# Performance work log

Measured on AMD Instinct MI355X. Metric: run time of the kernel, lower is better.

The kernel has to match this reference:

```python
import jax, jax.numpy as jnp
import numpy as np

N, HID, L, NC = 2048, 256, 4, 10
D0, D1, D2 = HID, HID // 2, HID // 8   # dims for degrees l=0,1,2
H, DH = 4, HID // 4                    # heads for degree-0 attention
F = D0 + D1 + D2                       # invariant feature width
C2 = float(np.sqrt(3.0))


def setup_inputs() -> dict:
    key = jax.random.key(0)
    ks = jax.random.split(key, 16)

    def w(k, shape, fan):
        return jax.random.normal(k, shape, jnp.float32) / np.float32(np.sqrt(fan))

    return {
        "x": jax.random.uniform(ks[0], (N, 118), jnp.float32),
        "pos": jax.random.normal(ks[1], (N, 3), jnp.float32) * 3.0,
        "emb_W": w(ks[2], (118, D0), 118),
        "emb_b": jnp.zeros((D0,), jnp.float32),
        "Wq": w(ks[3], (L, F, H * DH), F),
        "Wk": w(ks[4], (L, F, H * DH), F),
        "Wv0": w(ks[5], (L, D0, D0), D0),
        "Wv1": w(ks[6], (L, D1, D1), D1),
        "Wv2": w(ks[7], (L, D2, D2), D2),
        "Ws1": w(ks[8], (L, D0, D1), D0),
        "Ws2": w(ks[9], (L, D0, D2), D0),
        "Wffa": w(ks[10], (L, D0, 2 * D0), D0),
        "Wffb": w(ks[11], (L, 2 * D0, D0), 2 * D0),
        "Wg": w(ks[12], (L, F, D1 + D2), F),
        "out_W": w(ks[13], (D0, NC), D0),
        "out_b": jnp.zeros((NC,), jnp.float32),
    }


def _sph_harmonics(pos):
    """Real spherical harmonics Y1 [N,N,3], Y2 [N,N,5] of pairwise unit vectors."""
    rel = pos[None, :, :] - pos[:, None, :]                  # [N,N,3]
    dist = jnp.linalg.norm(rel, axis=-1, keepdims=True)
    valid = (dist > 1e-6).astype(pos.dtype)                  # zero out self-pairs
    u = rel / jnp.maximum(dist, 1e-6) * valid
    ux, uy, uz = u[..., 0], u[..., 1], u[..., 2]
    Y1 = u
    Y2 = jnp.stack([
        C2 * ux * uy,
        C2 * uy * uz,
        0.5 * (3.0 * uz * uz - 1.0),
        C2 * ux * uz,
        0.5 * C2 * (ux * ux - uy * uy),
    ], axis=-1) * valid                                      # [N,N,5]
    return Y1, Y2


def _invariants(x0, x1, x2):
    return jnp.concatenate([
        x0,
        jnp.linalg.norm(x1, axis=-1),
        jnp.linalg.norm(x2, axis=-1),
    ], axis=-1)                                              # [N,F]


def _layer(x0, x1, x2, Y1, Y2, Wq, Wk, Wv0, Wv1, Wv2, Ws1, Ws2, Wffa, Wffb, Wg):
    inv = _invariants(x0, x1, x2)
    q = (inv @ Wq).reshape(N, H, DH)
    k = (inv @ Wk).reshape(N, H, DH)
    attn = jax.nn.softmax(jnp.einsum('nhd,mhd->hnm', q, k) / np.float32(np.sqrt(DH)), axis=-1)

    # degree-0 aggregation (4 heads)
    v0 = (x0 @ Wv0).reshape(N, H, D0 // H)
    agg0 = jnp.einsum('hnm,mhc->nhc', attn, v0).reshape(N, D0)

    a = attn.mean(0)                                         # [N,N] single head for l>0
    # degree-1: channel-mixed values + degree-0 -> degree-1 via Y1
    v1 = jnp.einsum('mdc,de->mec', x1, Wv1)                  # [N,D1,3]
    agg1 = jnp.einsum('nm,mdc->ndc', a, v1)
    mix1 = jnp.einsum('nmc,md->ndc', a[:, :, None] * Y1, x0 @ Ws1)
    # degree-2: channel-mixed values + degree-0 -> degree-2 via Y2
    v2 = jnp.einsum('mdc,de->mec', x2, Wv2)                  # [N,D2,5]
    agg2 = jnp.einsum('nm,mdc->ndc', a, v2)
    mix2 = jnp.einsum('nmc,md->ndc', a[:, :, None] * Y2, x0 @ Ws2)

    x0 = x0 + agg0
    x1 = x1 + agg1 + mix1
    x2 = x2 + agg2 + mix2

    # gated equivariant feedforward
    x0 = x0 + jax.nn.silu(x0 @ Wffa) @ Wffb
    g = jax.nn.sigmoid(_invariants(x0, x1, x2) @ Wg)         # [N,D1+D2]
    x1 = x1 * g[:, :D1, None]
    x2 = x2 * g[:, D1:, None]
    return x0, x1, x2


def reference(x, pos, emb_W, emb_b, Wq, Wk, Wv0, Wv1, Wv2, Ws1, Ws2, Wffa, Wffb, Wg, out_W, out_b):
    Y1, Y2 = _sph_harmonics(pos)
    x0 = x @ emb_W + emb_b                                   # input embedding
    x1 = jnp.zeros((N, D1, 3), x0.dtype)
    x2 = jnp.zeros((N, D2, 5), x0.dtype)
    for l in range(L):
        x0, x1, x2 = _layer(x0, x1, x2, Y1, Y2,
                            Wq[l], Wk[l], Wv0[l], Wv1[l], Wv2[l],
                            Ws1[l], Ws2[l], Wffa[l], Wffb[l], Wg[l])
    return x0 @ out_W + out_b                                # [N, num_classes]
```

## Files before the change

### kernel.cpp

```cpp
#include <hip/hip_runtime.h>
#include <math.h>

#define N_    2048
#define D0_   256
#define D1_   128
#define D2_   32
#define F_    416
#define H_    4
#define DH_   64
#define L_    4
#define NC_   10
#define C2_   1.7320508075688772f
#define X12W  544

typedef unsigned short u16;
typedef __attribute__((ext_vector_type(8))) short short8v;
typedef __attribute__((ext_vector_type(4))) float f32x4;

union U8 { u16 u[8]; short8v v; };

__device__ __forceinline__ u16 f2bf(float f) {
    union { float f; unsigned int u; } x; x.f = f;
    unsigned int r = x.u + 0x7FFFu + ((x.u >> 16) & 1u);
    return (u16)(r >> 16);
}
__device__ __forceinline__ float bf2f(u16 u) {
    union { float f; unsigned int u; } x; x.u = ((unsigned int)u) << 16;
    return x.f;
}

__device__ __forceinline__ f32x4 mfma16(short8v a, short8v b, f32x4 c) {
    return __builtin_amdgcn_mfma_f32_16x16x32_bf16(a, b, c, 0, 0, 0);
}

enum { B_NN = 0, B_NT = 1 };
enum { EPI_STORE = 0, EPI_SILU = 1, EPI_SIGMOID = 2, EPI_ACCUM = 3, EPI_ATOMIC = 4,
       EPI_STOREB = 5 };

template<int BLAY, int EPI>
__global__ __launch_bounds__(256) void mfma_gemm(
    const float* __restrict__ A, int lda,
    const float* __restrict__ B, int ldb,
    const float* __restrict__ bias,
    float* __restrict__ C, int ldc,
    int M, int K, int Nn, float scale, int kchunk,
    int zk, long long Ah, long long Bh, long long Ch)
{
    __shared__ __align__(16) u16 As[64][40];
    __shared__ __align__(16) u16 Bs[64][40];
    const int t = threadIdx.x;
    const int bm = blockIdx.y * 64, bn = blockIdx.x * 64;
    const int hz = blockIdx.z / zk, kz = blockIdx.z % zk;
    A += (size_t)hz * Ah; B += (size_t)hz * Bh;
    const int lane = t & 63, w = t >> 6;
    const int r0 = (w >> 1) * 32, c0 = (w & 1) * 32;
    const int fr = lane & 15, fk = (lane >> 4) * 8;
    const int ml = t >> 2, k8 = (t & 3) * 8;
    const int kbeg = kz * kchunk;
    const int kend = (kbeg + kchunk < K) ? kbeg + kchunk : K;
    f32x4 acc[2][2] = {};

    for (int k0 = kbeg; k0 < kend; k0 += 32) {
        {
            U8 u;
            if (((lda & 3) == 0) && (k0 + 32 <= kend)) {
                const float* ap = A + (size_t)(bm + ml) * lda + k0 + k8;
                float4 a0 = *(const float4*)ap;
                float4 a1 = *(const float4*)(ap + 4);
                u.u[0]=f2bf(a0.x); u.u[1]=f2bf(a0.y); u.u[2]=f2bf(a0.z); u.u[3]=f2bf(a0.w);
                u.u[4]=f2bf(a1.x); u.u[5]=f2bf(a1.y); u.u[6]=f2bf(a1.z); u.u[7]=f2bf(a1.w);
            } else {
#pragma unroll
                for (int j = 0; j < 8; ++j) {
                    int kk = k0 + k8 + j;
                    u.u[j] = f2bf(kk < kend ? A[(size_t)(bm + ml) * lda + kk] : 0.f);
                }
            }
            *(short8v*)&As[ml][k8] = u.v;
        }
        {
            U8 u;
            if (BLAY == B_NT) {
                if (((ldb & 3) == 0) && (k0 + 32 <= kend) && (bn + ml < Nn)) {
                    const float* bp = B + (size_t)(bn + ml) * ldb + k0 + k8;
                    float4 b0 = *(const float4*)bp;
                    float4 b1 = *(const float4*)(bp + 4);
                    u.u[0]=f2bf(b0.x); u.u[1]=f2bf(b0.y); u.u[2]=f2bf(b0.z); u.u[3]=f2bf(b0.w);
                    u.u[4]=f2bf(b1.x); u.u[5]=f2bf(b1.y); u.u[6]=f2bf(b1.z); u.u[7]=f2bf(b1.w);
                } else {
#pragma unroll
                    for (int j = 0; j < 8; ++j) {
                        int kk = k0 + k8 + j;
                        u.u[j] = f2bf((kk < kend && bn + ml < Nn)
                                      ? B[(size_t)(bn + ml) * ldb + kk] : 0.f);
                    }
                }
            } else {
                int nc = bn + ml;
#pragma unroll
                for (int j = 0; j < 8; ++j) {
                    int kk = k0 + k8 + j;
                    u.u[j] = f2bf((kk < kend && nc < Nn) ? B[(size_t)kk * ldb + nc] : 0.f);
                }
            }
            *(short8v*)&Bs[ml][k8] = u.v;
        }
        __syncthreads();
        short8v a0 = *(const short8v*)&As[r0 + fr][fk];
        short8v a1 = *(const short8v*)&As[r0 + 16 + fr][fk];
        short8v b0 = *(const short8v*)&Bs[c0 + fr][fk];
        short8v b1 = *(const short8v*)&Bs[c0 + 16 + fr][fk];
        acc[0][0] = mfma16(a0, b0, acc[0][0]);
        acc[0][1] = mfma16(a0, b1, acc[0][1]);
        acc[1][0] = mfma16(a1, b0, acc[1][0]);
        acc[1][1] = mfma16(a1, b1, acc[1][1]);
        __syncthreads();
    }
#pragma unroll
    for (int mi = 0; mi < 2; ++mi)
#pragma unroll
    for (int ni = 0; ni < 2; ++ni)
#pragma unroll
    for (int r = 0; r < 4; ++r) {
        int row = bm + r0 + mi * 16 + ((lane >> 4) << 2) + r;
        int col = bn + c0 + ni * 16 + fr;
        if (col >= Nn) continue;
        float v = acc[mi][ni][r];
        if (EPI == EPI_STOREB) {
            ((u16*)C + (size_t)hz * Ch)[(size_t)row * ldc + col] = f2bf(v * scale);
        } else {
            float* cp = C + (size_t)hz * Ch + (size_t)row * ldc + col;
            if (EPI == EPI_STORE)   *cp = v * scale + (bias ? bias[col] : 0.f);
            if (EPI == EPI_SILU)    *cp = v / (1.f + expf(-v));
            if (EPI == EPI_SIGMOID) *cp = 1.f / (1.f + expf(-v));
            if (EPI == EPI_ACCUM)   *cp += v;
            if (EPI == EPI_ATOMIC)  atomicAdd(cp, v);
        }
    }
}

__global__ __launch_bounds__(256) void transpose_bf16(
    const float* __restrict__ in, u16* __restrict__ outT, int R, int C)
{
    __shared__ float tile[64][65];
    const int br = blockIdx.y * 64, bc = blockIdx.x * 64;
    const int t = threadIdx.x, lc = t & 63, q = t >> 6;
#pragma unroll 4
    for (int r = 0; r < 16; ++r) {
        int row = br + q * 16 + r, col = bc + lc;
        tile[q * 16 + r][lc] = (col < C) ? in[(size_t)row * C + col] : 0.f;
    }
    __syncthreads();
#pragma unroll 4
    for (int r = 0; r < 16; ++r) {
        int orow = bc + q * 16 + r;
        int ocol = br + lc;
        if (orow < C) outT[(size_t)orow * R + ocol] = f2bf(tile[lc][q * 16 + r]);
    }
}

template<int NB>
__global__ __launch_bounds__(256) void aggP(
    const u16* __restrict__ A, int lda,
    const u16* __restrict__ BT, int ldk,
    float* __restrict__ C, int ldc,
    int K, int Nn, int kchunk,
    int zk, long long Ah, long long Bh, long long Ch)
{
    __shared__ __align__(16) u16 As[64][40];
    __shared__ __align__(16) u16 Bs[NB][64][40];
    const int t = threadIdx.x;
    const int bm = blockIdx.y * 64, bn0 = blockIdx.x * 64 * NB;
    const int hz = blockIdx.z / zk, kz = blockIdx.z % zk;
    A += (size_t)hz * Ah; BT += (size_t)hz * Bh; C += (size_t)hz * Ch;
    const int lane = t & 63, w = t >> 6;
    const int r0 = (w >> 1) * 32, c0 = (w & 1) * 32;
    const int fr = lane & 15, fk = (lane >> 4) * 8;
    const int ml = t >> 2, k8 = (t & 3) * 8;
    const int kbeg = kz * kchunk;
    const int kend = (kbeg + kchunk < K) ? kbeg + kchunk : K;
    f32x4 acc[NB][2][2] = {};

    for (int k0 = kbeg; k0 < kend; k0 += 32) {
        *(short8v*)&As[ml][k8] = *(const short8v*)(A + (size_t)(bm + ml) * lda + k0 + k8);
#pragma unroll
        for (int nb = 0; nb < NB; ++nb) {
            int nc = bn0 + nb * 64 + ml;
            short8v z = {};
            *(short8v*)&Bs[nb][ml][k8] = (nc < Nn)
                ? *(const short8v*)(BT + (size_t)nc * ldk + k0 + k8) : z;
        }
        __syncthreads();
        short8v a0 = *(const short8v*)&As[r0 + fr][fk];
        short8v a1 = *(const short8v*)&As[r0 + 16 + fr][fk];
#pragma unroll
        for (int nb = 0; nb < NB; ++nb) {
            short8v b0 = *(const short8v*)&Bs[nb][c0 + fr][fk];
            short8v b1 = *(const short8v*)&Bs[nb][c0 + 16 + fr][fk];
            acc[nb][0][0] = mfma16(a0, b0, acc[nb][0][0]);
            acc[nb][0][1] = mfma16(a0, b1, acc[nb][0][1]);
            acc[nb][1][0] = mfma16(a1, b0, acc[nb][1][0]);
            acc[nb][1][1] = mfma16(a1, b1, acc[nb][1][1]);
        }
        __syncthreads();
    }
#pragma unroll
    for (int nb = 0; nb < NB; ++nb)
#pragma unroll
    for (int mi = 0; mi < 2; ++mi)
#pragma unroll
    for (int ni = 0; ni < 2; ++ni)
#pragma unroll
    for (int r = 0; r < 4; ++r) {
        int row = bm + r0 + mi * 16 + ((lane >> 4) << 2) + r;
        int col = bn0 + nb * 64 + c0 + ni * 16 + fr;
        if (col >= Nn) continue;
        atomicAdd(C + (size_t)row * ldc + col, acc[nb][mi][ni][r]);
    }
}

__global__ void ucompute_kernel(const float* __restrict__ pos, u16* __restrict__ U) {
    int idx = blockIdx.x * 256 + threadIdx.x;
    int n = idx >> 11, m = idx & (N_ - 1);
    float rx = pos[m * 3 + 0] - pos[n * 3 + 0];
    float ry = pos[m * 3 + 1] - pos[n * 3 + 1];
    float rz = pos[m * 3 + 2] - pos[n * 3 + 2];
    float d2 = rx * rx + ry * ry + rz * rz;
    bool valid = d2 > 1e-12f;
    float rinv = valid ? rsqrtf(d2) : 0.f;
    size_t base = (size_t)n * N_ + m;
    const size_t CS = (size_t)N_ * N_;
    U[base]          = f2bf(rx * rinv);
    U[base + CS]     = f2bf(ry * rinv);
    U[base + 2 * CS] = f2bf(rz * rinv);
}

__global__ __launch_bounds__(256) void mixc_kernel(
    const u16* __restrict__ amb, const u16* __restrict__ U,
    const u16* __restrict__ s1T, const u16* __restrict__ s2T,
    float* __restrict__ Macc)
{
    const int ch = blockIdx.z;
    const int gx = blockIdx.x;
    const bool deg1 = ch < 3;
    if (!deg1 && gx >= 8) return;
    const int bm = blockIdx.y * 64;
    const size_t CS = (size_t)N_ * N_;
    const int colbase = deg1 ? (gx & 1) * 64 : 0;
    const int ks      = deg1 ? (gx >> 1) : gx;
    const u16* BT     = deg1 ? s1T : s2T;
    __shared__ __align__(16) u16 As[64][40];
    __shared__ __align__(16) u16 Bs[64][40];
    const int t = threadIdx.x, lane = t & 63, w = t >> 6;
    const int r0 = (w >> 1) * 32, c0 = (w & 1) * 32;
    const int fr = lane & 15, fk = (lane >> 4) * 8;
    const int ml = t >> 2, k8 = (t & 3) * 8;
    const int kbeg = ks * 256, kend = kbeg + 256;
    f32x4 acc[2][2] = {};

    for (int m0 = kbeg; m0 < kend; m0 += 32) {
        const size_t off = (size_t)(bm + ml) * N_ + m0 + k8;
        U8 am8; am8.v = *(const short8v*)(amb + off);
        U8 o;
        if (deg1) {
            U8 uv; uv.v = *(const short8v*)(U + (size_t)ch * CS + off);
#pragma unroll
            for (int j = 0; j < 8; ++j)
                o.u[j] = f2bf(bf2f(am8.u[j]) * bf2f(uv.u[j]));
        } else {
            U8 xv, yv, zv;
            xv.v = *(const short8v*)(U + off);
            yv.v = *(const short8v*)(U + CS + off);
            zv.v = *(const short8v*)(U + 2 * CS + off);
#pragma unroll
            for (int j = 0; j < 8; ++j) {
                float a = bf2f(am8.u[j]);
                float ux = bf2f(xv.u[j]), uy = bf2f(yv.u[j]), uz = bf2f(zv.u[j]);
                float y;
                if      (ch == 3) y = C2_ * ux * uy;
                else if (ch == 4) y = C2_ * uy * uz;
                else if (ch == 5) y = (ux*ux + uy*uy + uz*uz > 0.5f)
                                      ? 0.5f * (3.f * uz * uz - 1.f) : 0.f;
                else if (ch == 6) y = C2_ * ux * uz;
                else              y = 0.5f * C2_ * (ux * ux - uy * uy);
                o.u[j] = f2bf(a * y);
            }
        }
        *(short8v*)&As[ml][k8] = o.v;
        {
            int nc = colbase + ml;
            short8v z = {};
            *(short8v*)&Bs[ml][k8] = (deg1 || nc < 32)
                ? *(const short8v*)(BT + (size_t)nc * N_ + m0 + k8) : z;
        }
        __syncthreads();
        short8v a0 = *(const short8v*)&As[r0 + fr][fk];
        short8v a1 = *(const short8v*)&As[r0 + 16 + fr][fk];
        short8v b0 = *(const short8v*)&Bs[c0 + fr][fk];
        short8v b1 = *(const short8v*)&Bs[c0 + 16 + fr][fk];
        acc[0][0] = mfma16(a0, b0, acc[0][0]);
        acc[0][1] = mfma16(a0, b1, acc[0][1]);
        acc[1][0] = mfma16(a1, b0, acc[1][0]);
        acc[1][1] = mfma16(a1, b1, acc[1][1]);
        __syncthreads();
    }
#pragma unroll
    for (int mi = 0; mi < 2; ++mi)
#pragma unroll
    for (int ni = 0; ni < 2; ++ni)
#pragma unroll
    for (int r = 0; r < 4; ++r) {
        int row = bm + r0 + mi * 16 + ((lane >> 4) << 2) + r;
        int col = colbase + c0 + ni * 16 + fr;
        float v = acc[mi][ni][r];
        if (deg1)
            atomicAdd(&Macc[(size_t)ch * N_ * 128 + (size_t)row * 128 + col], v);
        else if (col < 32)
            atomicAdd(&Macc[(size_t)3 * N_ * 128 + (size_t)(ch - 3) * N_ * 32
                            + (size_t)row * 32 + col], v);
    }
}

__global__ void mix_combine(const float* __restrict__ Macc, float* __restrict__ x12) {
    int idx = blockIdx.x * 256 + threadIdx.x;
    if (idx >= N_ * X12W) return;
    int n = idx / X12W, j = idx % X12W;
    float v;
    if (j < 384) {
        int e = j / 3, c = j - 3 * e;
        v = Macc[(size_t)c * N_ * 128 + (size_t)n * 128 + e];
    } else {
        int jj = j - 384;
        int e = jj / 5, c = jj - 5 * e;
        v = Macc[(size_t)3 * N_ * 128 + (size_t)c * N_ * 32 + (size_t)n * 32 + e];
    }
    x12[idx] += v;
}

__global__ void invar_kernel(const float* __restrict__ x0, const float* __restrict__ x12,
                             float* __restrict__ inv) {
    int n = blockIdx.x, t = threadIdx.x;
    inv[(size_t)n * F_ + t] = x0[(size_t)n * D0_ + t];
    if (t < 128) {
        const float* p = x12 + (size_t)n * X12W + t * 3;
        inv[(size_t)n * F_ + 256 + t] = sqrtf(p[0]*p[0] + p[1]*p[1] + p[2]*p[2]);
    }
    if (t < 32) {
        const float* p = x12 + (size_t)n * X12W + 384 + t * 5;
        inv[(size_t)n * F_ + 384 + t] =
            sqrtf(p[0]*p[0] + p[1]*p[1] + p[2]*p[2] + p[3]*p[3] + p[4]*p[4]);
    }
}

__global__ void v1_kernel(const float* __restrict__ x12, const float* __restrict__ W,
                          float* __restrict__ Vflat) {
    int m = blockIdx.x, t = threadIdx.x;
    __shared__ float sh[384];
    sh[t] = x12[(size_t)m * X12W + t];
    __syncthreads();
    int e = t / 3, c = t % 3;
    float acc = 0.f;
#pragma unroll 4
    for (int d = 0; d < 128; ++d)
        acc = fmaf(sh[d * 3 + c], W[d * 128 + e], acc);
    Vflat[(size_t)m * X12W + t] = acc;
}

__global__ void v2_kernel(const float* __restrict__ x12, const float* __restrict__ W,
                          float* __restrict__ Vflat) {
    int m = blockIdx.x, t = threadIdx.x;
    __shared__ float sh[160];
    if (t < 160) sh[t] = x12[(size_t)m * X12W + 384 + t];
    __syncthreads();
    if (t < 160) {
        int e = t / 5, c = t % 5;
        float acc = 0.f;
#pragma unroll 4
        for (int d = 0; d < 32; ++d)
            acc = fmaf(sh[d * 5 + c], W[d * 32 + e], acc);
        Vflat[(size_t)m * X12W + 384 + t] = acc;
    }
}

__global__ void softmax4(u16* __restrict__ Sb, u16* __restrict__ amb) {
    int n = blockIdx.x, t = threadIdx.x;
    __shared__ float red[256];
    const size_t NN = (size_t)N_ * N_;
    float amv[8] = {};
    for (int h = 0; h < H_; ++h) {
        u16* Sp = Sb + (size_t)h * NN + (size_t)n * N_ + t * 8;
        U8 sv; sv.v = *(const short8v*)Sp;
        float s[8];
#pragma unroll
        for (int j = 0; j < 8; ++j) s[j] = bf2f(sv.u[j]);
        float mx = s[0];
#pragma unroll
        for (int j = 1; j < 8; ++j) mx = fmaxf(mx, s[j]);
        red[t] = mx; __syncthreads();
        for (int st = 128; st > 0; st >>= 1) { if (t < st) red[t] = fmaxf(red[t], red[t + st]); __syncthreads(); }
        mx = red[0]; __syncthreads();
        float sum = 0.f;
#pragma unroll
        for (int j = 0; j < 8; ++j) { s[j] = expf(s[j] - mx); sum += s[j]; }
        red[t] = sum; __syncthreads();
        for (int st = 128; st > 0; st >>= 1) { if (t < st) red[t] += red[t + st]; __syncthreads(); }
        float rinv = 1.f / red[0]; __syncthreads();
        U8 pv;
#pragma unroll
        for (int j = 0; j < 8; ++j) {
            float p = s[j] * rinv;
            pv.u[j] = f2bf(p);
            amv[j] += 0.25f * p;
        }
        *(short8v*)Sp = pv.v;
    }
    U8 av;
#pragma unroll
    for (int j = 0; j < 8; ++j) av.u[j] = f2bf(amv[j]);
    *(short8v*)(amb + (size_t)n * N_ + t * 8) = av.v;
}

__global__ void gate_kernel(const float* __restrict__ g, float* __restrict__ x12) {
    int idx = blockIdx.x * 256 + threadIdx.x;
    if (idx >= N_ * X12W) return;
    int n = idx / X12W, j = idx % X12W;
    float gv = (j < 384) ? g[n * 160 + j / 3] : g[n * 160 + 128 + (j - 384) / 5];
    x12[idx] *= gv;
}

extern "C" void kernel_launch(void* const* d_in, const int* in_sizes, int n_in,
                              void* d_out, int out_size, void* d_ws, size_t ws_size,
                              hipStream_t stream) {
    const float* x    = (const float*)d_in[0];
    const float* pos  = (const float*)d_in[1];
    const float* embW = (const float*)d_in[2];
    const float* embB = (const float*)d_in[3];
    const float* Wq   = (const float*)d_in[4];
    const float* Wk   = (const float*)d_in[5];
    const float* Wv0  = (const float*)d_in[6];
    const float* Wv1  = (const float*)d_in[7];
    const float* Wv2  = (const float*)d_in[8];
    const float* Ws1  = (const float*)d_in[9];
    const float* Ws2  = (const float*)d_in[10];
    const float* Wffa = (const float*)d_in[11];
    const float* Wffb = (const float*)d_in[12];
    const float* Wg   = (const float*)d_in[13];
    const float* outW = (const float*)d_in[14];
    const float* outB = (const float*)d_in[15];
    float* out = (float*)d_out;

    const size_t NN = (size_t)N_ * N_;
    float* p = (float*)d_ws;
    float* x0    = p; p += N_ * D0_;
    float* x12   = p; p += N_ * X12W;
    float* inv   = p; p += N_ * F_;
    float* q     = p; p += N_ * D0_;
    float* k     = p; p += N_ * D0_;
    float* v0    = p; p += N_ * D0_;
    float* Vflat = p; p += N_ * X12W;
    float* s1    = p; p += N_ * D1_;
    float* s2    = p; p += N_ * D2_;
    float* fft   = p; p += N_ * 512;
    float* gm    = p; p += N_ * 160;
    float* Macc  = p; p += 3 * N_ * 128 + 5 * N_ * 32;
    u16* ub   = (u16*)p;
    u16* Sb   = ub; ub += 4 * NN;
    u16* amb  = ub; ub += NN;
    u16* U    = ub; ub += 3 * NN;
    u16* v0T  = ub; ub += D0_ * N_;
    u16* s1T  = ub; ub += D1_ * N_;
    u16* s2T  = ub; ub += D2_ * N_;
    u16* VflatT = ub; ub += X12W * N_;

    hipMemsetAsync(x12, 0, (size_t)N_ * X12W * sizeof(float), stream);
    ucompute_kernel<<<(N_ * N_) / 256, 256, 0, stream>>>(pos, U);

    mfma_gemm<B_NN, EPI_STORE><<<dim3(4, 32), 256, 0, stream>>>(
        x, 118, embW, 256, embB, x0, 256, N_, 118, 256, 1.f, 118, 1, 0, 0, 0);

    for (int l = 0; l < L_; ++l) {
        const float* Wq_l   = Wq   + (size_t)l * F_ * 256;
        const float* Wk_l   = Wk   + (size_t)l * F_ * 256;
        const float* Wv0_l  = Wv0  + (size_t)l * 256 * 256;
        const float* Wv1_l  = Wv1  + (size_t)l * 128 * 128;
        const float* Wv2_l  = Wv2  + (size_t)l * 32 * 32;
        const float* Ws1_l  = Ws1  + (size_t)l * 256 * 128;
        const float* Ws2_l  = Ws2  + (size_t)l * 256 * 32;
        const float* Wffa_l = Wffa + (size_t)l * 256 * 512;
        const float* Wffb_l = Wffb + (size_t)l * 512 * 256;
        const float* Wg_l   = Wg   + (size_t)l * F_ * 160;

        hipMemsetAsync(Macc, 0, (3 * N_ * 128 + 5 * N_ * 32) * sizeof(float), stream);
        invar_kernel<<<N_, 256, 0, stream>>>(x0, x12, inv);
        mfma_gemm<B_NN, EPI_STORE><<<dim3(4, 32), 256, 0, stream>>>(
            inv, F_, Wq_l, 256, nullptr, q, 256, N_, F_, 256, 1.f, F_, 1, 0, 0, 0);
        mfma_gemm<B_NN, EPI_STORE><<<dim3(4, 32), 256, 0, stream>>>(
            inv, F_, Wk_l, 256, nullptr, k, 256, N_, F_, 256, 1.f, F_, 1, 0, 0, 0);
        mfma_gemm<B_NN, EPI_STORE><<<dim3(4, 32), 256, 0, stream>>>(
            x0, 256, Wv0_l, 256, nullptr, v0, 256, N_, 256, 256, 1.f, 256, 1, 0, 0, 0);
        mfma_gemm<B_NN, EPI_STORE><<<dim3(2, 32), 256, 0, stream>>>(
            x0, 256, Ws1_l, 128, nullptr, s1, 128, N_, 256, 128, 1.f, 256, 1, 0, 0, 0);
        mfma_gemm<B_NN, EPI_STORE><<<dim3(1, 32), 256, 0, stream>>>(
            x0, 256, Ws2_l, 32, nullptr, s2, 32, N_, 256, 32, 1.f, 256, 1, 0, 0, 0);
        v1_kernel<<<N_, 384, 0, stream>>>(x12, Wv1_l, Vflat);
        v2_kernel<<<N_, 192, 0, stream>>>(x12, Wv2_l, Vflat);

        transpose_bf16<<<dim3(4, 32), 256, 0, stream>>>(v0, v0T, N_, 256);
        transpose_bf16<<<dim3(2, 32), 256, 0, stream>>>(s1, s1T, N_, 128);
        transpose_bf16<<<dim3(1, 32), 256, 0, stream>>>(s2, s2T, N_, 32);
        transpose_bf16<<<dim3(9, 32), 256, 0, stream>>>(Vflat, VflatT, N_, X12W);

        mfma_gemm<B_NT, EPI_STOREB><<<dim3(32, 32, 4), 256, 0, stream>>>(
            q, 256, k, 256, nullptr, (float*)Sb, N_, N_, 64, N_, 0.125f, 64,
            1, 64, 64, (long long)NN);
        softmax4<<<N_, 256, 0, stream>>>(Sb, amb);
        aggP<1><<<dim3(1, 32, 32), 256, 0, stream>>>(
            Sb, N_, v0T, N_, x0, 256, N_, 64, 256,
            8, (long long)NN, (long long)(64 * N_), 64);

        aggP<3><<<dim3(3, 32, 4), 256, 0, stream>>>(
            amb, N_, VflatT, N_, x12, X12W, N_, X12W, 512,
            4, 0, 0, 0);
        mixc_kernel<<<dim3(16, 32, 8), 256, 0, stream>>>(amb, U, s1T, s2T, Macc);
        mix_combine<<<(N_ * X12W + 255) / 256, 256, 0, stream>>>(Macc, x12);

        mfma_gemm<B_NN, EPI_SILU><<<dim3(8, 32), 256, 0, stream>>>(
            x0, 256, Wffa_l, 512, nullptr, fft, 512, N_, 256, 512, 1.f, 256, 1, 0, 0, 0);
        mfma_gemm<B_NN, EPI_ACCUM><<<dim3(4, 32), 256, 0, stream>>>(
            fft, 512, Wffb_l, 256, nullptr, x0, 256, N_, 512, 256, 1.f, 512, 1, 0, 0, 0);

        invar_kernel<<<N_, 256, 0, stream>>>(x0, x12, inv);
        mfma_gemm<B_NN, EPI_SIGMOID><<<dim3(3, 32), 256, 0, stream>>>(
            inv, F_, Wg_l, 160, nullptr, gm, 160, N_, F_, 160, 1.f, F_, 1, 0, 0, 0);
        gate_kernel<<<(N_ * X12W + 255) / 256, 256, 0, stream>>>(gm, x12);
    }

    mfma_gemm<B_NN, EPI_STORE><<<dim3(1, 32), 256, 0, stream>>>(
        x0, 256, outW, NC_, outB, out, NC_, N_, 256, NC_, 1.f, 256, 1, 0, 0, 0);
}
```

Before: 1.484 ms.

## Fuse spherical-harmonic channels in mix kernel to reuse loaded tiles

Splits the mix kernel into per-degree template instances that compute all 3 (degree-1) or 5 (degree-2) harmonic channels in one block. Each block loads the attention-mean and unit-vector tiles once and reuses the shared B tile across channels, where before every channel block reloaded them. This adds more accumulators and LDS per block, which may lower occupancy, and the launch grid is reshaped. The softmax kernel is only moved within the file.

```diff
diff --git a/kernel.cpp b/kernel.cpp
--- a/kernel.cpp
+++ b/kernel.cpp
@@ -28,7 +28,6 @@
     union { float f; unsigned int u; } x; x.u = ((unsigned int)u) << 16;
     return x.f;
 }
-
 __device__ __forceinline__ f32x4 mfma16(short8v a, short8v b, f32x4 c) {
     return __builtin_amdgcn_mfma_f32_16x16x32_bf16(a, b, c, 0, 0, 0);
 }
@@ -235,75 +234,81 @@
     U[base + 2 * CS] = f2bf(rz * rinv);
 }
 
-__global__ __launch_bounds__(256) void mixc_kernel(
+template<int DEG>
+__global__ __launch_bounds__(256) void mixf_kernel(
     const u16* __restrict__ amb, const u16* __restrict__ U,
-    const u16* __restrict__ s1T, const u16* __restrict__ s2T,
-    float* __restrict__ Macc)
+    const u16* __restrict__ BT, float* __restrict__ Macc, int kchunk)
 {
-    const int ch = blockIdx.z;
-    const int gx = blockIdx.x;
-    const bool deg1 = ch < 3;
-    if (!deg1 && gx >= 8) return;
+    constexpr int NCH = (DEG == 1) ? 3 : 5;
     const int bm = blockIdx.y * 64;
+    const int colbase = blockIdx.z * 64;
     const size_t CS = (size_t)N_ * N_;
-    const int colbase = deg1 ? (gx & 1) * 64 : 0;
-    const int ks      = deg1 ? (gx >> 1) : gx;
-    const u16* BT     = deg1 ? s1T : s2T;
-    __shared__ __align__(16) u16 As[64][40];
+    __shared__ __align__(16) u16 As[NCH][64][40];
     __shared__ __align__(16) u16 Bs[64][40];
     const int t = threadIdx.x, lane = t & 63, w = t >> 6;
     const int r0 = (w >> 1) * 32, c0 = (w & 1) * 32;
     const int fr = lane & 15, fk = (lane >> 4) * 8;
     const int ml = t >> 2, k8 = (t & 3) * 8;
-    const int kbeg = ks * 256, kend = kbeg + 256;
-    f32x4 acc[2][2] = {};
+    const int kbeg = blockIdx.x * kchunk, kend = kbeg + kchunk;
+    f32x4 acc[NCH][2][2] = {};
 
     for (int m0 = kbeg; m0 < kend; m0 += 32) {
         const size_t off = (size_t)(bm + ml) * N_ + m0 + k8;
         U8 am8; am8.v = *(const short8v*)(amb + off);
-        U8 o;
-        if (deg1) {
-            U8 uv; uv.v = *(const short8v*)(U + (size_t)ch * CS + off);
-#pragma unroll
-            for (int j = 0; j < 8; ++j)
-                o.u[j] = f2bf(bf2f(am8.u[j]) * bf2f(uv.u[j]));
+        U8 xv, yv, zv;
+        xv.v = *(const short8v*)(U + off);
+        yv.v = *(const short8v*)(U + CS + off);
+        zv.v = *(const short8v*)(U + 2 * CS + off);
+        if (DEG == 1) {
+            U8 o0, o1, o2;
+#pragma unroll
+            for (int j = 0; j < 8; ++j) {
+                float a = bf2f(am8.u[j]);
+                o0.u[j] = f2bf(a * bf2f(xv.u[j]));
+                o1.u[j] = f2bf(a * bf2f(yv.u[j]));
+                o2.u[j] = f2bf(a * bf2f(zv.u[j]));
+            }
+            *(short8v*)&As[0][ml][k8] = o0.v;
+            *(short8v*)&As[1][ml][k8] = o1.v;
+            *(short8v*)&As[2][ml][k8] = o2.v;
         } else {
-            U8 xv, yv, zv;
-            xv.v = *(const short8v*)(U + off);
-            yv.v = *(const short8v*)(U + CS + off);
-            zv.v = *(const short8v*)(U + 2 * CS + off);
+            U8 o[5];
 #pragma unroll
             for (int j = 0; j < 8; ++j) {
                 float a = bf2f(am8.u[j]);
                 float ux = bf2f(xv.u[j]), uy = bf2f(yv.u[j]), uz = bf2f(zv.u[j]);
-                float y;
-                if      (ch == 3) y = C2_ * ux * uy;
-                else if (ch == 4) y = C2_ * uy * uz;
-                else if (ch == 5) y = (ux*ux + uy*uy + uz*uz > 0.5f)
-                                      ? 0.5f * (3.f * uz * uz - 1.f) : 0.f;
-                else if (ch == 6) y = C2_ * ux * uz;
-                else              y = 0.5f * C2_ * (ux * ux - uy * uy);
-                o.u[j] = f2bf(a * y);
+                o[0].u[j] = f2bf(a * C2_ * ux * uy);
+                o[1].u[j] = f2bf(a * C2_ * uy * uz);
+                o[2].u[j] = f2bf((ux*ux + uy*uy + uz*uz > 0.5f)
+                                 ? a * 0.5f * (3.f * uz * uz - 1.f) : 0.f);
+                o[3].u[j] = f2bf(a * C2_ * ux * uz);
+                o[4].u[j] = f2bf(a * 0.5f * C2_ * (ux * ux - uy * uy));
             }
-        }
-        *(short8v*)&As[ml][k8] = o.v;
+#pragma unroll
+            for (int c = 0; c < 5; ++c) *(short8v*)&As[c][ml][k8] = o[c].v;
+        }
         {
             int nc = colbase + ml;
             short8v z = {};
-            *(short8v*)&Bs[ml][k8] = (deg1 || nc < 32)
+            *(short8v*)&Bs[ml][k8] = (DEG == 1 || nc < 32)
                 ? *(const short8v*)(BT + (size_t)nc * N_ + m0 + k8) : z;
         }
         __syncthreads();
-        short8v a0 = *(const short8v*)&As[r0 + fr][fk];
-        short8v a1 = *(const short8v*)&As[r0 + 16 + fr][fk];
         short8v b0 = *(const short8v*)&Bs[c0 + fr][fk];
         short8v b1 = *(const short8v*)&Bs[c0 + 16 + fr][fk];
-        acc[0][0] = mfma16(a0, b0, acc[0][0]);
-        acc[0][1] = mfma16(a0, b1, acc[0][1]);
-        acc[1][0] = mfma16(a1, b0, acc[1][0]);
-        acc[1][1] = mfma16(a1, b1, acc[1][1]);
+#pragma unroll
+        for (int c = 0; c < NCH; ++c) {
+            short8v a0 = *(const short8v*)&As[c][r0 + fr][fk];
+            short8v a1 = *(const short8v*)&As[c][r0 + 16 + fr][fk];
+            acc[c][0][0] = mfma16(a0, b0, acc[c][0][0]);
+            acc[c][0][1] = mfma16(a0, b1, acc[c][0][1]);
+            acc[c][1][0] = mfma16(a1, b0, acc[c][1][0]);
+            acc[c][1][1] = mfma16(a1, b1, acc[c][1][1]);
+        }
         __syncthreads();
     }
+#pragma unroll
+    for (int c = 0; c < NCH; ++c)
 #pragma unroll
     for (int mi = 0; mi < 2; ++mi)
 #pragma unroll
@@ -312,11 +317,11 @@
     for (int r = 0; r < 4; ++r) {
         int row = bm + r0 + mi * 16 + ((lane >> 4) << 2) + r;
         int col = colbase + c0 + ni * 16 + fr;
-        float v = acc[mi][ni][r];
-        if (deg1)
-            atomicAdd(&Macc[(size_t)ch * N_ * 128 + (size_t)row * 128 + col], v);
+        float v = acc[c][mi][ni][r];
+        if (DEG == 1)
+            atomicAdd(&Macc[(size_t)c * N_ * 128 + (size_t)row * 128 + col], v);
         else if (col < 32)
-            atomicAdd(&Macc[(size_t)3 * N_ * 128 + (size_t)(ch - 3) * N_ * 32
+            atomicAdd(&Macc[(size_t)3 * N_ * 128 + (size_t)c * N_ * 32
                             + (size_t)row * 32 + col], v);
     }
 }
@@ -335,6 +340,44 @@
         v = Macc[(size_t)3 * N_ * 128 + (size_t)c * N_ * 32 + (size_t)n * 32 + e];
     }
     x12[idx] += v;
+}
+
+__global__ void softmax4(u16* __restrict__ Sb, u16* __restrict__ amb) {
+    int n = blockIdx.x, t = threadIdx.x;
+    __shared__ float red[256];
+    const size_t NN = (size_t)N_ * N_;
+    float amv[8] = {};
+    for (int h = 0; h < H_; ++h) {
+        u16* Sp = Sb + (size_t)h * NN + (size_t)n * N_ + t * 8;
+        U8 sv; sv.v = *(const short8v*)Sp;
+        float s[8];
+#pragma unroll
+        for (int j = 0; j < 8; ++j) s[j] = bf2f(sv.u[j]);
+        float mx = s[0];
+#pragma unroll
+        for (int j = 1; j < 8; ++j) mx = fmaxf(mx, s[j]);
+        red[t] = mx; __syncthreads();
+        for (int st = 128; st > 0; st >>= 1) { if (t < st) red[t] = fmaxf(red[t], red[t + st]); __syncthreads(); }
+        mx = red[0]; __syncthreads();
+        float sum = 0.f;
+#pragma unroll
+        for (int j = 0; j < 8; ++j) { s[j] = expf(s[j] - mx); sum += s[j]; }
+        red[t] = sum; __syncthreads();
+        for (int st = 128; st > 0; st >>= 1) { if (t < st) red[t] += red[t + st]; __syncthreads(); }
+        float rinv = 1.f / red[0]; __syncthreads();
+        U8 pv;
+#pragma unroll
+        for (int j = 0; j < 8; ++j) {
+            float p = s[j] * rinv;
+            pv.u[j] = f2bf(p);
+            amv[j] += 0.25f * p;
+        }
+        *(short8v*)Sp = pv.v;
+    }
+    U8 av;
+#pragma unroll
+    for (int j = 0; j < 8; ++j) av.u[j] = f2bf(amv[j]);
+    *(short8v*)(amb + (size_t)n * N_ + t * 8) = av.v;
 }
 
 __global__ void invar_kernel(const float* __restrict__ x0, const float* __restrict__ x12,
@@ -380,44 +423,6 @@
             acc = fmaf(sh[d * 5 + c], W[d * 32 + e], acc);
         Vflat[(size_t)m * X12W + 384 + t] = acc;
     }
-}
-
-__global__ void softmax4(u16* __restrict__ Sb, u16* __restrict__ amb) {
-    int n = blockIdx.x, t = threadIdx.x;
-    __shared__ float red[256];
-    const size_t NN = (size_t)N_ * N_;
-    float amv[8] = {};
-    for (int h = 0; h < H_; ++h) {
-        u16* Sp = Sb + (size_t)h * NN + (size_t)n * N_ + t * 8;
-        U8 sv; sv.v = *(const short8v*)Sp;
-        float s[8];
-#pragma unroll
-        for (int j = 0; j < 8; ++j) s[j] = bf2f(sv.u[j]);
-        float mx = s[0];
-#pragma unroll
-        for (int j = 1; j < 8; ++j) mx = fmaxf(mx, s[j]);
-        red[t] = mx; __syncthreads();
-        for (int st = 128; st > 0; st >>= 1) { if (t < st) red[t] = fmaxf(red[t], red[t + st]); __syncthreads(); }
-        mx = red[0]; __syncthreads();
-        float sum = 0.f;
-#pragma unroll
-        for (int j = 0; j < 8; ++j) { s[j] = expf(s[j] - mx); sum += s[j]; }
-        red[t] = sum; __syncthreads();
-        for (int st = 128; st > 0; st >>= 1) { if (t < st) red[t] += red[t + st]; __syncthreads(); }
-        float rinv = 1.f / red[0]; __syncthreads();
-        U8 pv;
-#pragma unroll
-        for (int j = 0; j < 8; ++j) {
-            float p = s[j] * rinv;
-            pv.u[j] = f2bf(p);
-            amv[j] += 0.25f * p;
-        }
-        *(short8v*)Sp = pv.v;
-    }
-    U8 av;
-#pragma unroll
-    for (int j = 0; j < 8; ++j) av.u[j] = f2bf(amv[j]);
-    *(short8v*)(amb + (size_t)n * N_ + t * 8) = av.v;
 }
 
 __global__ void gate_kernel(const float* __restrict__ g, float* __restrict__ x12) {
@@ -521,7 +526,8 @@
         aggP<3><<<dim3(3, 32, 4), 256, 0, stream>>>(
             amb, N_, VflatT, N_, x12, X12W, N_, X12W, 512,
             4, 0, 0, 0);
-        mixc_kernel<<<dim3(16, 32, 8), 256, 0, stream>>>(amb, U, s1T, s2T, Macc);
+        mixf_kernel<1><<<dim3(8, 32, 2), 256, 0, stream>>>(amb, U, s1T, Macc, 256);
+        mixf_kernel<2><<<dim3(16, 32, 1), 256, 0, stream>>>(amb, U, s2T, Macc, 128);
         mix_combine<<<(N_ * X12W + 255) / 256, 256, 0, stream>>>(Macc, x12);
 
         mfma_gemm<B_NN, EPI_SILU><<<dim3(8, 32), 256, 0, stream>>>(
```

Result: no change. 1.463 ms (-1.4%).
